# Kernel tuning notes

Measured on AMD Instinct MI355X. Metric: run time of the kernel, lower is better.

## Reference

```python
import jax, jax.numpy as jnp
import numpy as np


def setup_inputs() -> dict:
    key = jax.random.key(0)
    k1, k2 = jax.random.split(key)
    X = jax.random.normal(k1, (8192, 3), dtype=jnp.float32)
    Y = jax.random.normal(k2, (8192, 3), dtype=jnp.float32)
    return {"X": X, "Y": Y}


def reference(X, Y):
    # Pairwise L2 distances: torch.norm(x - y) for every (x, y) pair.
    # d[i, j] = ||X[i] - Y[j]||_2, shape [N, M]
    diff = X[:, None, :] - Y[None, :, :]          # [N, M, D]
    d = jnp.sqrt(jnp.sum(diff * diff, axis=-1))   # [N, M]
    hd_xy = jnp.max(jnp.min(d, axis=1))           # max over x of min over y
    hd_yx = jnp.max(jnp.min(d, axis=0))           # max over y of min over x
    return jnp.maximum(hd_xy, hd_yx)
```

## Files before the change

### kernel.cpp

```cpp
#include <hip/hip_runtime.h>
#include <math.h>


typedef float v2f __attribute__((ext_vector_type(2)));

constexpr int NPTS = 8192;
constexpr int T = 256;
constexpr int R = 4;
constexpr int ROWS_PB = T * R;
constexpr int RG = NPTS / ROWS_PB;
constexpr int CG = 32;
constexpr int COLS = NPTS / CG;

constexpr int RT = 64;
constexpr int RBLK = 2 * NPTS / RT;

__global__ __launch_bounds__(T) void pair_partial_kernel(
        const float* __restrict__ X, const float* __restrict__ Y,
        float* __restrict__ partial, unsigned* __restrict__ counter) {
    int b = blockIdx.x;
    if (b == 0 && threadIdx.x == 0) *counter = 0u;
    int dir = b / (RG * CG);
    int rem = b - dir * (RG * CG);
    int rg = rem / CG;
    int cg = rem - rg * CG;
    const float* A = dir ? Y : X;
    const float* B = dir ? X : Y;

    int t = threadIdx.x;
    int r0 = rg * ROWS_PB + t;

    v2f ax2[R / 2], ay2[R / 2], az2[R / 2], na2[R / 2], mt2[R / 2];
#pragma unroll
    for (int q = 0; q < R / 2; ++q) {
        int ra = r0 + (2 * q) * T;
        int rb = r0 + (2 * q + 1) * T;
        ax2[q] = (v2f){A[ra * 3 + 0], A[rb * 3 + 0]};
        ay2[q] = (v2f){A[ra * 3 + 1], A[rb * 3 + 1]};
        az2[q] = (v2f){A[ra * 3 + 2], A[rb * 3 + 2]};
    }

    __shared__ float4 Bs[COLS];
    for (int i = t; i < COLS; i += T) {
        int j = cg * COLS + i;
        float bx = B[j * 3 + 0], by = B[j * 3 + 1], bz = B[j * 3 + 2];
        Bs[i] = make_float4(bx, by, bz, -0.5f * fmaf(bx, bx, fmaf(by, by, bz * bz)));
    }

#pragma unroll
    for (int q = 0; q < R / 2; ++q) {
        na2[q] = ax2[q] * ax2[q] + ay2[q] * ay2[q] + az2[q] * az2[q];
        mt2[q] = (v2f){-__builtin_inff(), -__builtin_inff()};
    }
    __syncthreads();

#pragma unroll 8
    for (int j = 0; j < COLS; ++j) {
        float4 p = Bs[j];
        v2f px = (v2f){p.x, p.x};
        v2f py = (v2f){p.y, p.y};
        v2f pz = (v2f){p.z, p.z};
        v2f pw = (v2f){p.w, p.w};
#pragma unroll
        for (int q = 0; q < R / 2; ++q) {
            v2f tt = az2[q] * pz + pw;
            tt = ay2[q] * py + tt;
            tt = ax2[q] * px + tt;
            mt2[q] = __builtin_elementwise_max(mt2[q], tt);
        }
    }

    float* op = partial + (size_t)(dir * CG + cg) * NPTS + rg * ROWS_PB + t;
#pragma unroll
    for (int q = 0; q < R / 2; ++q) {
        op[(2 * q) * T]     = fmaf(-2.f, mt2[q].x, na2[q].x);
        op[(2 * q + 1) * T] = fmaf(-2.f, mt2[q].y, na2[q].y);
    }
}

__global__ __launch_bounds__(RT) void reduce_final_kernel(
        const float* __restrict__ partial, float* __restrict__ blockmax,
        unsigned* __restrict__ counter, float* __restrict__ out) {
    int rid = blockIdx.x * RT + threadIdx.x;
    int dir = rid >> 13;
    int row = rid & (NPTS - 1);
    const float* p = partial + (size_t)dir * CG * NPTS + row;

    float m[8];
#pragma unroll
    for (int k = 0; k < 8; ++k) m[k] = __builtin_inff();
#pragma unroll
    for (int cg = 0; cg < CG; ++cg)
        m[cg & 7] = fminf(m[cg & 7], p[(size_t)cg * NPTS]);
#pragma unroll
    for (int k = 0; k < 4; ++k) m[k] = fminf(m[k], m[k + 4]);
    float mm = fmaxf(fminf(fminf(m[0], m[1]), fminf(m[2], m[3])), 0.f);

#pragma unroll
    for (int o = 32; o > 0; o >>= 1) mm = fmaxf(mm, __shfl_xor(mm, o));
    if (threadIdx.x == 0)
        __hip_atomic_store(&blockmax[blockIdx.x], mm, __ATOMIC_RELEASE,
                           __HIP_MEMORY_SCOPE_AGENT);

    __shared__ unsigned is_last;
    if (threadIdx.x == 0)
        is_last = (__hip_atomic_fetch_add(counter, 1u, __ATOMIC_ACQ_REL,
                                          __HIP_MEMORY_SCOPE_AGENT) == RBLK - 1);
    __syncthreads();
    if (!is_last) return;

    float bm = 0.f;
#pragma unroll
    for (int k = 0; k < RBLK / RT; ++k) {
        float v = __hip_atomic_load(&blockmax[k * RT + threadIdx.x],
                                    __ATOMIC_ACQUIRE, __HIP_MEMORY_SCOPE_AGENT);
        bm = fmaxf(bm, v);
    }
#pragma unroll
    for (int o = 32; o > 0; o >>= 1) bm = fmaxf(bm, __shfl_xor(bm, o));
    if (threadIdx.x == 0) out[0] = sqrtf(bm);
}


__global__ void init_min_kernel(unsigned* wsmin, int n) {
    int i = blockIdx.x * blockDim.x + threadIdx.x;
    if (i < n) wsmin[i] = 0x7F800000u;
}

__global__ __launch_bounds__(256) void pair_min_kernel(
        const float* __restrict__ X, const float* __restrict__ Y,
        unsigned* __restrict__ minXY, unsigned* __restrict__ minYX) {
    constexpr int SEG_J = 512;
    constexpr int SEGS = NPTS / SEG_J;
    constexpr int RPB8 = 256 * 8;
    constexpr int BLOCKS_PER_DIR = (NPTS / RPB8) * SEGS;
    int b = blockIdx.x;
    int dir = b / BLOCKS_PER_DIR;
    int rem = b - dir * BLOCKS_PER_DIR;
    int rg = rem / SEGS;
    int seg = rem - rg * SEGS;
    const float* A = dir ? Y : X;
    const float* B = dir ? X : Y;
    unsigned* omin = dir ? minYX : minXY;

    __shared__ float Bs[SEG_J * 3];
    int t = threadIdx.x;
    const float* Bseg = B + seg * SEG_J * 3;
    for (int i = t; i < SEG_J * 3; i += 256) Bs[i] = Bseg[i];

    int r0 = rg * RPB8 + t;
    float ax[8], ay[8], az[8], m[8];
#pragma unroll
    for (int r = 0; r < 8; ++r) {
        int row = r0 + r * 256;
        ax[r] = A[row * 3 + 0];
        ay[r] = A[row * 3 + 1];
        az[r] = A[row * 3 + 2];
        m[r] = __builtin_inff();
    }
    __syncthreads();

#pragma unroll 2
    for (int j = 0; j < SEG_J; ++j) {
        float bx = Bs[3 * j + 0], by = Bs[3 * j + 1], bz = Bs[3 * j + 2];
#pragma unroll
        for (int r = 0; r < 8; ++r) {
            float dx = ax[r] - bx, dy = ay[r] - by, dz = az[r] - bz;
            m[r] = fminf(m[r], fmaf(dx, dx, fmaf(dy, dy, dz * dz)));
        }
    }
#pragma unroll
    for (int r = 0; r < 8; ++r)
        atomicMin(&omin[r0 + r * 256], __float_as_uint(m[r]));
}

__global__ __launch_bounds__(256) void finalize_min_kernel(
        const unsigned* __restrict__ wsmin, float* __restrict__ out, int n) {
    int t = threadIdx.x;
    float mx = 0.f;
    for (int i = t; i < n; i += 256) mx = fmaxf(mx, __uint_as_float(wsmin[i]));
    for (int o = 32; o > 0; o >>= 1) mx = fmaxf(mx, __shfl_down(mx, o));
    __shared__ float wmax[4];
    if ((t & 63) == 0) wmax[t >> 6] = mx;
    __syncthreads();
    if (t == 0) {
        float mm = fmaxf(fmaxf(wmax[0], wmax[1]), fmaxf(wmax[2], wmax[3]));
        out[0] = sqrtf(mm);
    }
}

extern "C" void kernel_launch(void* const* d_in, const int* in_sizes, int n_in,
                              void* d_out, int out_size, void* d_ws, size_t ws_size,
                              hipStream_t stream) {
    const float* X = (const float*)d_in[0];
    const float* Y = (const float*)d_in[1];
    float* out = (float*)d_out;

    const size_t partial_elems = (size_t)2 * CG * NPTS;
    const size_t need = (partial_elems + RBLK + 1) * sizeof(float);

    if (ws_size >= need) {
        float* partial = (float*)d_ws;
        float* blockmax = partial + partial_elems;
        unsigned* counter = (unsigned*)(blockmax + RBLK);
        pair_partial_kernel<<<2 * RG * CG, T, 0, stream>>>(X, Y, partial, counter);
        reduce_final_kernel<<<RBLK, RT, 0, stream>>>(partial, blockmax, counter, out);
    } else if (ws_size >= 2 * NPTS * sizeof(unsigned)) {
        unsigned* wsmin = (unsigned*)d_ws;
        init_min_kernel<<<(2 * NPTS + 255) / 256, 256, 0, stream>>>(wsmin, 2 * NPTS);
        pair_min_kernel<<<2 * (NPTS / (256 * 8)) * (NPTS / 512), 256, 0, stream>>>(
            X, Y, wsmin, wsmin + NPTS);
        finalize_min_kernel<<<1, 256, 0, stream>>>(wsmin, out, 2 * NPTS);
    }
}
```

Before: 28.49 us.

## Compute pairwise dot products with split-bf16 MFMA instead of FP32 VALU loops

Packs each point into hi/lo bf16 parts, with the -0.5·|b|² term folded in, so a single 32x32x16 bf16 MFMA yields a·b − 0.5|b|² at near-fp32 precision. The per-row max is kept in registers across all columns, then reduced across lanes and waves in one block, and a small final kernel takes the global max. This replaces the partial-buffer write and the atomic-counter reduction. It adds a prep kernel and a third launch, and the split-bf16 products drop the lo×lo term, so small accuracy errors are possible.

Measured after the change: 27.37 us. 3.9% less time.

```diff
diff --git a/kernel.cpp b/kernel.cpp
--- a/kernel.cpp
+++ b/kernel.cpp
@@ -2,123 +2,131 @@
 #include <math.h>
 
 
-typedef float v2f __attribute__((ext_vector_type(2)));
+typedef __attribute__((ext_vector_type(8))) short bf16x8;
+typedef __attribute__((ext_vector_type(16))) float f32x16;
+typedef __attribute__((ext_vector_type(4))) unsigned uint4v;
 
 constexpr int NPTS = 8192;
-constexpr int T = 256;
-constexpr int R = 4;
-constexpr int ROWS_PB = T * R;
-constexpr int RG = NPTS / ROWS_PB;
-constexpr int CG = 32;
-constexpr int COLS = NPTS / CG;
-
-constexpr int RT = 64;
-constexpr int RBLK = 2 * NPTS / RT;
-
-__global__ __launch_bounds__(T) void pair_partial_kernel(
+
+static __device__ __forceinline__ unsigned short f2bf_rn(float x) {
+    unsigned u = __float_as_uint(x);
+    unsigned r = u + 0x7FFFu + ((u >> 16) & 1u);
+    return (unsigned short)(r >> 16);
+}
+
+__global__ __launch_bounds__(256) void prep_kernel(
         const float* __restrict__ X, const float* __restrict__ Y,
-        float* __restrict__ partial, unsigned* __restrict__ counter) {
+        unsigned short* __restrict__ Apack, unsigned short* __restrict__ Bpack) {
+    int i = blockIdx.x * 256 + threadIdx.x;
+    const float* src = (i < NPTS) ? (X + (size_t)i * 3) : (Y + (size_t)(i - NPTS) * 3);
+    float x0 = src[0], x1 = src[1], x2 = src[2];
+
+    unsigned short h0 = f2bf_rn(x0), h1 = f2bf_rn(x1), h2 = f2bf_rn(x2);
+    float hf0 = __uint_as_float((unsigned)h0 << 16);
+    float hf1 = __uint_as_float((unsigned)h1 << 16);
+    float hf2 = __uint_as_float((unsigned)h2 << 16);
+    unsigned short l0 = f2bf_rn(x0 - hf0);
+    unsigned short l1 = f2bf_rn(x1 - hf1);
+    unsigned short l2 = f2bf_rn(x2 - hf2);
+
+    float c = -0.5f * fmaf(x0, x0, fmaf(x1, x1, x2 * x2));
+    unsigned short ch = f2bf_rn(c);
+    float chf = __uint_as_float((unsigned)ch << 16);
+    unsigned short cl = f2bf_rn(c - chf);
+
+    const unsigned short ONE = 0x3F80;
+    alignas(16) unsigned short a[16] = {h0, h1, h2, h0, h1, h2, l0, l1,
+                                        l2, ONE, ONE, 0, 0, 0, 0, 0};
+    alignas(16) unsigned short bb[16] = {h0, h1, h2, l0, l1, l2, h0, h1,
+                                         h2, ch, cl, 0, 0, 0, 0, 0};
+
+    unsigned short* ap = Apack + (size_t)i * 16;
+    unsigned short* bp = Bpack + (size_t)(i ^ NPTS) * 16;
+    *(uint4v*)(ap)     = *(const uint4v*)(a);
+    *(uint4v*)(ap + 8) = *(const uint4v*)(a + 8);
+    *(uint4v*)(bp)     = *(const uint4v*)(bb);
+    *(uint4v*)(bp + 8) = *(const uint4v*)(bb + 8);
+}
+
+__global__ __launch_bounds__(256) void mfma_main_kernel(
+        const float* __restrict__ X, const float* __restrict__ Y,
+        const unsigned short* __restrict__ Apack,
+        const unsigned short* __restrict__ Bpack,
+        float* __restrict__ d2buf) {
     int b = blockIdx.x;
-    if (b == 0 && threadIdx.x == 0) *counter = 0u;
-    int dir = b / (RG * CG);
-    int rem = b - dir * (RG * CG);
-    int rg = rem / CG;
-    int cg = rem - rg * CG;
-    const float* A = dir ? Y : X;
-    const float* B = dir ? X : Y;
-
-    int t = threadIdx.x;
-    int r0 = rg * ROWS_PB + t;
-
-    v2f ax2[R / 2], ay2[R / 2], az2[R / 2], na2[R / 2], mt2[R / 2];
-#pragma unroll
-    for (int q = 0; q < R / 2; ++q) {
-        int ra = r0 + (2 * q) * T;
-        int rb = r0 + (2 * q + 1) * T;
-        ax2[q] = (v2f){A[ra * 3 + 0], A[rb * 3 + 0]};
-        ay2[q] = (v2f){A[ra * 3 + 1], A[rb * 3 + 1]};
-        az2[q] = (v2f){A[ra * 3 + 2], A[rb * 3 + 2]};
-    }
-
-    __shared__ float4 Bs[COLS];
-    for (int i = t; i < COLS; i += T) {
-        int j = cg * COLS + i;
-        float bx = B[j * 3 + 0], by = B[j * 3 + 1], bz = B[j * 3 + 2];
-        Bs[i] = make_float4(bx, by, bz, -0.5f * fmaf(bx, bx, fmaf(by, by, bz * bz)));
-    }
-
-#pragma unroll
-    for (int q = 0; q < R / 2; ++q) {
-        na2[q] = ax2[q] * ax2[q] + ay2[q] * ay2[q] + az2[q] * az2[q];
-        mt2[q] = (v2f){-__builtin_inff(), -__builtin_inff()};
-    }
-    __syncthreads();
-
-#pragma unroll 8
-    for (int j = 0; j < COLS; ++j) {
-        float4 p = Bs[j];
-        v2f px = (v2f){p.x, p.x};
-        v2f py = (v2f){p.y, p.y};
-        v2f pz = (v2f){p.z, p.z};
-        v2f pw = (v2f){p.w, p.w};
-#pragma unroll
-        for (int q = 0; q < R / 2; ++q) {
-            v2f tt = az2[q] * pz + pw;
-            tt = ay2[q] * py + tt;
-            tt = ax2[q] * px + tt;
-            mt2[q] = __builtin_elementwise_max(mt2[q], tt);
-        }
-    }
-
-    float* op = partial + (size_t)(dir * CG + cg) * NPTS + rg * ROWS_PB + t;
-#pragma unroll
-    for (int q = 0; q < R / 2; ++q) {
-        op[(2 * q) * T]     = fmaf(-2.f, mt2[q].x, na2[q].x);
-        op[(2 * q + 1) * T] = fmaf(-2.f, mt2[q].y, na2[q].y);
-    }
-}
-
-__global__ __launch_bounds__(RT) void reduce_final_kernel(
-        const float* __restrict__ partial, float* __restrict__ blockmax,
-        unsigned* __restrict__ counter, float* __restrict__ out) {
-    int rid = blockIdx.x * RT + threadIdx.x;
-    int dir = rid >> 13;
-    int row = rid & (NPTS - 1);
-    const float* p = partial + (size_t)dir * CG * NPTS + row;
-
-    float m[8];
-#pragma unroll
-    for (int k = 0; k < 8; ++k) m[k] = __builtin_inff();
-#pragma unroll
-    for (int cg = 0; cg < CG; ++cg)
-        m[cg & 7] = fminf(m[cg & 7], p[(size_t)cg * NPTS]);
-#pragma unroll
-    for (int k = 0; k < 4; ++k) m[k] = fminf(m[k], m[k + 4]);
-    float mm = fmaxf(fminf(fminf(m[0], m[1]), fminf(m[2], m[3])), 0.f);
-
-#pragma unroll
-    for (int o = 32; o > 0; o >>= 1) mm = fmaxf(mm, __shfl_xor(mm, o));
-    if (threadIdx.x == 0)
-        __hip_atomic_store(&blockmax[blockIdx.x], mm, __ATOMIC_RELEASE,
-                           __HIP_MEMORY_SCOPE_AGENT);
-
-    __shared__ unsigned is_last;
-    if (threadIdx.x == 0)
-        is_last = (__hip_atomic_fetch_add(counter, 1u, __ATOMIC_ACQ_REL,
-                                          __HIP_MEMORY_SCOPE_AGENT) == RBLK - 1);
-    __syncthreads();
-    if (!is_last) return;
-
-    float bm = 0.f;
-#pragma unroll
-    for (int k = 0; k < RBLK / RT; ++k) {
-        float v = __hip_atomic_load(&blockmax[k * RT + threadIdx.x],
-                                    __ATOMIC_ACQUIRE, __HIP_MEMORY_SCOPE_AGENT);
-        bm = fmaxf(bm, v);
-    }
-#pragma unroll
-    for (int o = 32; o > 0; o >>= 1) bm = fmaxf(bm, __shfl_xor(bm, o));
-    if (threadIdx.x == 0) out[0] = sqrtf(bm);
+    int dir = b >> 8;
+    int row0 = (b & 255) * 32;
+    int t = threadIdx.x;
+    int w = t >> 6, l = t & 63;
+    int lhalf = l >> 5, lmod = l & 31;
+
+    bf16x8 af = *(const bf16x8*)(Apack +
+        ((size_t)(dir * NPTS + row0 + lmod) * 16 + lhalf * 8));
+
+    const unsigned short* Bbase = Bpack +
+        ((size_t)(dir * NPTS + w * 2048 + lmod) * 16 + lhalf * 8);
+
+    f32x16 rmax;
+#pragma unroll
+    for (int r = 0; r < 16; ++r) rmax[r] = -__builtin_inff();
+    f32x16 zacc;
+#pragma unroll
+    for (int r = 0; r < 16; ++r) zacc[r] = 0.f;
+
+#pragma unroll 2
+    for (int tile = 0; tile < 64; ++tile) {
+        bf16x8 bf = *(const bf16x8*)(Bbase + (size_t)tile * 32 * 16);
+        f32x16 d = __builtin_amdgcn_mfma_f32_32x32x16_bf16(af, bf, zacc, 0, 0, 0);
+#pragma unroll
+        for (int r = 0; r < 16; ++r) rmax[r] = fmaxf(rmax[r], d[r]);
+    }
+
+#pragma unroll
+    for (int o = 1; o <= 16; o <<= 1) {
+#pragma unroll
+        for (int r = 0; r < 16; ++r)
+            rmax[r] = fmaxf(rmax[r], __shfl_xor(rmax[r], o));
+    }
+
+    __shared__ float rmaxs[4][32];
+    if (lmod == 0) {
+#pragma unroll
+        for (int r = 0; r < 16; ++r)
+            rmaxs[w][(r & 3) + 8 * (r >> 2) + 4 * lhalf] = rmax[r];
+    }
+    __syncthreads();
+
+    if (t < 32) {
+        float m = fmaxf(fmaxf(rmaxs[0][t], rmaxs[1][t]),
+                        fmaxf(rmaxs[2][t], rmaxs[3][t]));
+        int row = row0 + t;
+        const float* A = dir ? Y : X;
+        float a0 = A[(size_t)row * 3 + 0];
+        float a1 = A[(size_t)row * 3 + 1];
+        float a2 = A[(size_t)row * 3 + 2];
+        float na = fmaf(a0, a0, fmaf(a1, a1, a2 * a2));
+        d2buf[dir * NPTS + row] = fmaxf(fmaf(-2.f, m, na), 0.f);
+    }
+}
+
+__global__ __launch_bounds__(1024) void final_kernel(
+        const float* __restrict__ d2buf, float* __restrict__ out) {
+    int t = threadIdx.x;
+    float m = 0.f;
+#pragma unroll
+    for (int k = 0; k < 2 * NPTS / 1024; ++k)
+        m = fmaxf(m, d2buf[k * 1024 + t]);
+#pragma unroll
+    for (int o = 32; o > 0; o >>= 1) m = fmaxf(m, __shfl_xor(m, o));
+    __shared__ float wm[16];
+    if ((t & 63) == 0) wm[t >> 6] = m;
+    __syncthreads();
+    if (t == 0) {
+        float mm = wm[0];
+#pragma unroll
+        for (int v = 1; v < 16; ++v) mm = fmaxf(mm, wm[v]);
+        out[0] = sqrtf(mm);
+    }
 }
 
 
@@ -196,15 +204,17 @@
     const float* Y = (const float*)d_in[1];
     float* out = (float*)d_out;
 
-    const size_t partial_elems = (size_t)2 * CG * NPTS;
-    const size_t need = (partial_elems + RBLK + 1) * sizeof(float);
+    const size_t pack_elems = (size_t)2 * NPTS * 16;
+    const size_t apack_b = pack_elems * sizeof(unsigned short);
+    const size_t need = 2 * apack_b + (size_t)2 * NPTS * sizeof(float) + 256;
 
     if (ws_size >= need) {
-        float* partial = (float*)d_ws;
-        float* blockmax = partial + partial_elems;
-        unsigned* counter = (unsigned*)(blockmax + RBLK);
-        pair_partial_kernel<<<2 * RG * CG, T, 0, stream>>>(X, Y, partial, counter);
-        reduce_final_kernel<<<RBLK, RT, 0, stream>>>(partial, blockmax, counter, out);
+        unsigned short* Apack = (unsigned short*)d_ws;
+        unsigned short* Bpack = Apack + pack_elems;
+        float* d2buf = (float*)(Bpack + pack_elems);
+        prep_kernel<<<2 * NPTS / 256, 256, 0, stream>>>(X, Y, Apack, Bpack);
+        mfma_main_kernel<<<512, 256, 0, stream>>>(X, Y, Apack, Bpack, d2buf);
+        final_kernel<<<1, 1024, 0, stream>>>(d2buf, out);
     } else if (ws_size >= 2 * NPTS * sizeof(unsigned)) {
         unsigned* wsmin = (unsigned*)d_ws;
         init_min_kernel<<<(2 * NPTS + 255) / 256, 256, 0, stream>>>(wsmin, 2 * NPTS);
```
